# Kernel tuning notes

Hardware: AMD Instinct MI355X
Metric: run time of the kernel (lower is better)

Reference implementation:

```python
import jax, jax.numpy as jnp
import numpy as np

D_MODEL = 2048
N_HEADS = 16
D_HEAD = D_MODEL // N_HEADS  # 128
RANK = 32


def _orthogonal(key, rows, cols, dtype=jnp.float32):
    # mimic torch orthogonal init via QR
    a = jax.random.normal(key, (max(rows, cols), min(rows, cols)), dtype=jnp.float32)
    q, r = jnp.linalg.qr(a)
    q = q * jnp.sign(jnp.diagonal(r))
    if rows < cols:
        q = q.T
    return q.astype(dtype)


def setup_inputs() -> dict:
    key = jax.random.key(0)
    ks = jax.random.split(key, 8)
    B, T = 2, 2048
    x = jax.random.normal(ks[0], (B, T, D_MODEL), dtype=jnp.float32)
    s = 1.0 / np.sqrt(D_MODEL)
    Wq = jax.random.uniform(ks[1], (D_MODEL, D_MODEL), minval=-s, maxval=s, dtype=jnp.float32)
    Wk = jax.random.uniform(ks[2], (D_MODEL, D_MODEL), minval=-s, maxval=s, dtype=jnp.float32)
    Wv = jax.random.uniform(ks[3], (D_MODEL, D_MODEL), minval=-s, maxval=s, dtype=jnp.float32)
    Wo = jax.random.uniform(ks[4], (D_MODEL, D_MODEL), minval=-s, maxval=s, dtype=jnp.float32)
    # vein projector: project d_head -> rank, reconstruct rank -> d_head (orthogonal init)
    Wdown = _orthogonal(ks[5], D_HEAD, RANK)   # [d_head, r]
    Wup = _orthogonal(ks[6], RANK, D_HEAD)     # [r, d_head]
    return {"x": x, "Wq": Wq, "Wk": Wk, "Wv": Wv, "Wo": Wo, "Wdown": Wdown, "Wup": Wup}


def reference(x, Wq, Wk, Wv, Wo, Wdown, Wup):
    B, T, D = x.shape
    H, dh, r = N_HEADS, D_HEAD, RANK
    scale = 1.0 / np.sqrt(r)

    def heads(y):  # [B,T,D] -> [B,H,T,dh]
        return y.reshape(B, T, H, dh).transpose(0, 2, 1, 3)

    q = heads(x @ Wq.T)
    k = heads(x @ Wk.T)
    v = heads(x @ Wv.T)

    # project into vein (rank) space: [B,H,T,r]
    q_r = jnp.einsum('bhtd,dr->bhtr', q, Wdown)
    k_r = jnp.einsum('bhtd,dr->bhtr', k, Wdown)
    v_r = jnp.einsum('bhtd,dr->bhtr', v, Wdown)

    scores = jnp.einsum('bhqr,bhkr->bhqk', q_r, k_r) * scale  # [B,H,T,T]
    attn = jax.nn.softmax(scores, axis=-1)
    y_r = jnp.einsum('bhqk,bhkr->bhqr', attn, v_r)            # [B,H,T,r]
    y = jnp.einsum('bhtr,rd->bhtd', y_r, Wup)                  # reconstruct [B,H,T,dh]
    y = y.transpose(0, 2, 1, 3).reshape(B, T, D)
    out = y @ Wo.T
    return out
```

## Files before the change

kernel.cpp:

```cpp
#include <hip/hip_runtime.h>
#include <cstdint>
#include <cstddef>

typedef __bf16 bf16;
typedef __attribute__((ext_vector_type(8))) __bf16 bf16x8;
typedef __attribute__((ext_vector_type(4))) __bf16 bf16x4;
typedef __attribute__((ext_vector_type(2))) __bf16 bf16x2;
typedef __attribute__((ext_vector_type(4))) float f32x4;
typedef unsigned int u32;

#define D_MODEL 2048
#define QSCALE      0.17677669529663687f
#define QSCALE_L2E  (0.17677669529663687f * 1.4426950408889634f)

__device__ inline void async_load16(const void* gp, void* lp) {
  __builtin_amdgcn_global_load_lds(
      (const __attribute__((address_space(1))) u32*)gp,
      (__attribute__((address_space(3))) u32*)lp, 16, 0, 0);
}

__device__ inline float fast_exp2(float x) {
#if __has_builtin(__builtin_amdgcn_exp2f)
  return __builtin_amdgcn_exp2f(x);
#else
  return __expf(x * 0.6931471805599453f);
#endif
}

__device__ inline bf16x8 cvt8(float4 a, float4 b) {
  bf16x8 o;
  o[0] = (bf16)a.x; o[1] = (bf16)a.y; o[2] = (bf16)a.z; o[3] = (bf16)a.w;
  o[4] = (bf16)b.x; o[5] = (bf16)b.y; o[6] = (bf16)b.z; o[7] = (bf16)b.w;
  return o;
}

__global__ __launch_bounds__(256) void prep_k(
    const float* __restrict__ x,  const float* __restrict__ Wq,
    const float* __restrict__ Wk, const float* __restrict__ Wv,
    const float* __restrict__ Wo, const float* __restrict__ Wdown,
    const float* __restrict__ Wup,
    bf16* __restrict__ xb, bf16* __restrict__ EffT,
    bf16* __restrict__ WoEffT) {
  __shared__ __align__(16) char smem_[24576];
  const int bid = blockIdx.x;
  const int t = threadIdx.x;

  if (bid < 768) {
    const int mh = bid % 48;
    const int dblk = bid / 48;
    const float* W = (mh < 16) ? Wq : ((mh < 32) ? Wk : Wv);
    const int hrow = (mh & 15) * 128;
    const int d = dblk * 128 + (t & 127);
    const int rh = (t >> 7) * 16;
    const int rhs = __builtin_amdgcn_readfirstlane(rh);
    const float* wdn = Wdown + rhs;
    float acc[16];
#pragma unroll
    for (int j = 0; j < 16; ++j) acc[j] = 0.f;
    for (int kb = 0; kb < 16; ++kb) {
      float wv[8];
#pragma unroll
      for (int u = 0; u < 8; ++u)
        wv[u] = W[(size_t)(hrow + kb * 8 + u) * D_MODEL + d];
#pragma unroll
      for (int u = 0; u < 8; ++u) {
#pragma unroll
        for (int j = 0; j < 16; ++j)
          acc[j] += wv[u] * wdn[(kb * 8 + u) * 32 + j];
      }
    }
    bf16* outp = EffT + (size_t)(mh * 32 + rh) * D_MODEL + d;
#pragma unroll
    for (int j = 0; j < 16; ++j) outp[(size_t)j * D_MODEL] = (bf16)acc[j];
    return;
  }

  if (bid >= 1280) {
    const int tid = (bid - 1280) * 256 + t;
    float4 v[8];
#pragma unroll
    for (int p = 0; p < 4; ++p) {
      const int i = (tid + p * 262144) * 8;
      v[2 * p]     = *(const float4*)(x + i);
      v[2 * p + 1] = *(const float4*)(x + i + 4);
    }
#pragma unroll
    for (int p = 0; p < 4; ++p) {
      const int i = (tid + p * 262144) * 8;
      *(bf16x8*)(xb + i) = cvt8(v[2 * p], v[2 * p + 1]);
    }
    return;
  }

  bf16* As_ = (bf16*)smem_;
  bf16* Bs_ = (bf16*)(smem_ + 16384);
  const int rel = bid - 768;
  const int d0 = (rel & 31) * 64, h = rel >> 5;
  const int wave = t >> 6, lane = t & 63;
  const int quad = lane >> 4, lc = lane & 15;
#pragma unroll
  for (int a = 0; a < 4; ++a) {
    int cc = a * 256 + t;
    int row = cc >> 4, c = cc & 15;
    const float* src = Wo + (size_t)(d0 + row) * 2048 + h * 128 + c * 8;
    float4 f0 = ((const float4*)src)[0], f1 = ((const float4*)src)[1];
    *(bf16x8*)(As_ + row * 128 + ((c ^ (row & 15)) * 8)) = cvt8(f0, f1);
  }
  {
    int row = t >> 3;
    int c0 = (t & 7) * 2;
    const float* src = Wup + row * 128 + c0 * 8;
    float4 f0 = ((const float4*)src)[0], f1 = ((const float4*)src)[1];
    float4 f2 = ((const float4*)src)[2], f3 = ((const float4*)src)[3];
    *(bf16x8*)(Bs_ + row * 128 + ((c0 ^ (row & 15)) * 8)) = cvt8(f0, f1);
    *(bf16x8*)(Bs_ + row * 128 + (((c0 + 1) ^ (row & 15)) * 8)) = cvt8(f2, f3);
  }
  __syncthreads();
  f32x4 acc[2] = {};
  const int wm = wave * 16;
#pragma unroll
  for (int kc = 0; kc < 4; ++kc) {
    int m = wm + lc;
    bf16x8 af = *(const bf16x8*)(As_ + m * 128 + (((kc * 4 + quad) ^ (m & 15)) * 8));
#pragma unroll
    for (int ni = 0; ni < 2; ++ni) {
      int n = ni * 16 + lc;
      bf16x8 bfr = *(const bf16x8*)(Bs_ + n * 128 + (((kc * 4 + quad) ^ (n & 15)) * 8));
      acc[ni] = __builtin_amdgcn_mfma_f32_16x16x32_bf16(af, bfr, acc[ni], 0, 0, 0);
    }
  }
#pragma unroll
  for (int ni = 0; ni < 2; ++ni)
#pragma unroll
    for (int reg = 0; reg < 4; ++reg)
      WoEffT[(size_t)(d0 + wm + quad * 4 + reg) * 512 + h * 32 +
             ni * 16 + lc] = (bf16)acc[ni][reg];
}

template <int EPI, int BM>
__global__ __launch_bounds__(256, (BM == 64 ? 3 : 2)) void gemm_bt_k(
    const bf16* __restrict__ A, const bf16* __restrict__ Bt,
    void* __restrict__ Cv, int M, int N, int K) {
  constexpr int MI = BM / 32;
  constexpr int AR = BM / 4;
  __shared__ __align__(16) bf16 As[2][BM * 64];
  __shared__ __align__(16) bf16 Bs[2][128 * 64];
  const int t = threadIdx.x, wave = t >> 6, lane = t & 63;
  const int quad = lane >> 4, lc = lane & 15;
  const size_t m0 = (size_t)blockIdx.x * BM;
  const size_t n0 = (size_t)blockIdx.y * 128;
  const int wm = (wave >> 1) * (MI * 16), wn = (wave & 1) * 64;
  const int sr = lane >> 3, ss = lane & 7;
  const bf16* Aga[MI]; const bf16* Bga[4]; int LoffA[MI], LoffB[4];
#pragma unroll
  for (int a = 0; a < MI; ++a) {
    int row = wave * AR + a * 8 + sr;
    Aga[a] = A + (m0 + row) * (size_t)K + (ss ^ (row & 7)) * 8;
    LoffA[a] = (wave * AR + a * 8) * 64;
  }
#pragma unroll
  for (int a = 0; a < 4; ++a) {
    int row = wave * 32 + a * 8 + sr;
    Bga[a] = Bt + (n0 + row) * (size_t)K + (ss ^ (row & 7)) * 8;
    LoffB[a] = (wave * 32 + a * 8) * 64;
  }
  f32x4 acc[MI][4] = {};
  const int NIT = K >> 6;
#pragma unroll
  for (int a = 0; a < MI; ++a) async_load16(Aga[a], &As[0][LoffA[a]]);
#pragma unroll
  for (int a = 0; a < 4; ++a) async_load16(Bga[a], &Bs[0][LoffB[a]]);
  __syncthreads();
  for (int it = 0; it < NIT; ++it) {
    const int cur = it & 1;
    if (it + 1 < NIT) {
      const int k0 = (it + 1) * 64;
#pragma unroll
      for (int a = 0; a < MI; ++a) async_load16(Aga[a] + k0, &As[1 - cur][LoffA[a]]);
#pragma unroll
      for (int a = 0; a < 4; ++a) async_load16(Bga[a] + k0, &Bs[1 - cur][LoffB[a]]);
    }
    const bf16* Asb = As[cur];
    const bf16* Bsb = Bs[cur];
#pragma unroll
    for (int kc = 0; kc < 2; ++kc) {
      bf16x8 af[MI], bfr[4];
#pragma unroll
      for (int mi = 0; mi < MI; ++mi) {
        int m = wm + mi * 16 + lc;
        af[mi] = *(const bf16x8*)(Asb + m * 64 + (((kc * 4 + quad) ^ (m & 7)) * 8));
      }
#pragma unroll
      for (int ni = 0; ni < 4; ++ni) {
        int n = wn + ni * 16 + lc;
        bfr[ni] = *(const bf16x8*)(Bsb + n * 64 + (((kc * 4 + quad) ^ (n & 7)) * 8));
      }
#pragma unroll
      for (int mi = 0; mi < MI; ++mi)
#pragma unroll
        for (int ni = 0; ni < 4; ++ni)
          acc[mi][ni] = __builtin_amdgcn_mfma_f32_16x16x32_bf16(
              af[mi], bfr[ni], acc[mi][ni], 0, 0, 0);
    }
    __syncthreads();
  }

  if (EPI == 0) {
    float* C = (float*)Cv;
#pragma unroll
    for (int mi = 0; mi < MI; ++mi)
#pragma unroll
      for (int ni = 0; ni < 4; ++ni) {
        size_t row = m0 + wm + mi * 16 + quad * 4;
        size_t col = n0 + wn + ni * 16 + lc;
#pragma unroll
        for (int reg = 0; reg < 4; ++reg)
          C[(row + reg) * (size_t)N + col] = acc[mi][ni][reg];
      }
  } else {
    bf16* C = (bf16*)Cv;
#pragma unroll
    for (int mi = 0; mi < MI; ++mi)
#pragma unroll
      for (int ni = 0; ni < 4; ++ni) {
        int n = (int)n0 + wn + ni * 16 + lc;
        int mat = n >> 9, hh = (n >> 5) & 15, r = n & 31;
        float sc = (mat == 0) ? QSCALE_L2E : 1.0f;
        int trow = (int)m0 + wm + mi * 16 + quad * 4;
        int b = trow >> 11, tl = trow & 2047;
        if (mat == 2) {
          int tile = tl >> 7, kin = tl & 127;
          size_t off = ((size_t)(b * 16 + hh) * 3 + 2) * 65536 +
                       (size_t)tile * 4096 + r * 128 +
                       (((kin >> 3) ^ (r & 15)) << 3) + (kin & 7);
          bf16x4 pk;
#pragma unroll
          for (int reg = 0; reg < 4; ++reg) pk[reg] = (bf16)acc[mi][ni][reg];
          *(bf16x4*)(C + off) = pk;
        } else {
#pragma unroll
          for (int reg = 0; reg < 4; ++reg) {
            size_t off = (((size_t)(b * 16 + hh) * 3 + mat) * 2048 + tl + reg) * 32 + r;
            C[off] = (bf16)(acc[mi][ni][reg] * sc);
          }
        }
      }
  }
}

__global__ __launch_bounds__(256, 4) void attn_k(const bf16* __restrict__ QKVr,
                                                 float* __restrict__ Op,
                                                 float* __restrict__ Sums) {
  const int bh = blockIdx.x, qb = blockIdx.y, kvh = blockIdx.z;
  const size_t base = (size_t)bh * 3 * 65536;
  const bf16* Q   = QKVr + base;
  const bf16* Kr  = Q + 65536 + (size_t)kvh * 1024 * 32;
  const bf16* Vrb = Q + 131072 + (size_t)kvh * 8 * 4096;
  __shared__ __align__(16) bf16 Ks[2][128 * 32];
  __shared__ __align__(16) bf16 Vt[2][32 * 128];
  __shared__ __align__(16) bf16 Ps[4 * 32 * 32];
  const int t = threadIdx.x, wave = t >> 6, lane = t & 63;
  const int quad = lane >> 4, lc = lane & 15;
  const int qbase = qb * 128 + wave * 32;
  const bf16x8 qf0 = *(const bf16x8*)(Q + (size_t)(qbase + lc) * 32 + quad * 8);
  const bf16x8 qf1 = *(const bf16x8*)(Q + (size_t)(qbase + 16 + lc) * 32 + quad * 8);
  f32x4 o00 = {}, o01 = {}, o10 = {}, o11 = {};
  f32x4 os0 = {}, os1 = {};
  bf16x8 ones;
#pragma unroll
  for (int j = 0; j < 8; ++j) ones[j] = (bf16)1.0f;
  const int krow = wave * 16 + (lane >> 2);
  const bf16* Kg = Kr + (size_t)krow * 32 + ((lane & 3) ^ ((krow >> 1) & 3)) * 8;
  bf16* pw = Ps + wave * 32 * 32;
  const int psw = (lc & 3) ^ (lc >> 2);

  async_load16(Kg, &Ks[0][wave * 16 * 32]);
  async_load16(Kg + (size_t)64 * 32, &Ks[0][(64 + wave * 16) * 32]);
  async_load16(Vrb + (wave * 2) * 512 + lane * 8, &Vt[0][(wave * 2) * 512]);
  async_load16(Vrb + (wave * 2 + 1) * 512 + lane * 8, &Vt[0][(wave * 2 + 1) * 512]);
  __syncthreads();

  for (int it = 0; it < 8; ++it) {
    const int kt = it * 128, cur = it & 1;
    if (it < 7) {
      async_load16(Kg + (size_t)(kt + 128) * 32, &Ks[1 - cur][wave * 16 * 32]);
      async_load16(Kg + (size_t)(kt + 192) * 32, &Ks[1 - cur][(64 + wave * 16) * 32]);
      const bf16* vg = Vrb + (size_t)(it + 1) * 4096;
      async_load16(vg + (wave * 2) * 512 + lane * 8, &Vt[1 - cur][(wave * 2) * 512]);
      async_load16(vg + (wave * 2 + 1) * 512 + lane * 8, &Vt[1 - cur][(wave * 2 + 1) * 512]);
    }
    const bf16* ksb = Ks[cur];
    const bf16* vtb = Vt[cur];
#pragma unroll
    for (int qtr = 0; qtr < 4; ++qtr) {
#pragma unroll
      for (int nii = 0; nii < 2; ++nii) {
        int ni = qtr * 2 + nii;
        int n = ni * 16 + lc;
        bf16x8 kf = *(const bf16x8*)(ksb + n * 32 + ((quad ^ ((n >> 1) & 3)) * 8));
        f32x4 z = {0.f, 0.f, 0.f, 0.f};
        f32x4 s0 = __builtin_amdgcn_mfma_f32_16x16x32_bf16(kf, qf0, z, 0, 0, 0);
        f32x4 s1 = __builtin_amdgcn_mfma_f32_16x16x32_bf16(kf, qf1, z, 0, 0, 0);
        bf16x4 p0, p1;
#pragma unroll
        for (int reg = 0; reg < 4; ++reg) {
          p0[reg] = (bf16)fast_exp2(s0[reg]);
          p1[reg] = (bf16)fast_exp2(s1[reg]);
        }
        int off = (((2 * nii + (quad >> 1)) ^ psw) * 8) + (quad & 1) * 4;
        *(bf16x4*)(pw + lc * 32 + off) = p0;
        *(bf16x4*)(pw + (16 + lc) * 32 + off) = p1;
      }
      int co = (quad ^ psw) * 8;
      bf16x8 pf0 = *(const bf16x8*)(pw + lc * 32 + co);
      bf16x8 pf1 = *(const bf16x8*)(pw + (16 + lc) * 32 + co);
      int vo = ((qtr * 4 + quad) ^ lc) * 8;
      bf16x8 v0 = *(const bf16x8*)(vtb + lc * 128 + vo);
      bf16x8 v1 = *(const bf16x8*)(vtb + (16 + lc) * 128 + vo);
      o00 = __builtin_amdgcn_mfma_f32_16x16x32_bf16(pf0, v0, o00, 0, 0, 0);
      o01 = __builtin_amdgcn_mfma_f32_16x16x32_bf16(pf0, v1, o01, 0, 0, 0);
      o10 = __builtin_amdgcn_mfma_f32_16x16x32_bf16(pf1, v0, o10, 0, 0, 0);
      o11 = __builtin_amdgcn_mfma_f32_16x16x32_bf16(pf1, v1, o11, 0, 0, 0);
      os0 = __builtin_amdgcn_mfma_f32_16x16x32_bf16(pf0, ones, os0, 0, 0, 0);
      os1 = __builtin_amdgcn_mfma_f32_16x16x32_bf16(pf1, ones, os1, 0, 0, 0);
    }
    __syncthreads();
  }
  const int b = bh >> 4, h = bh & 15;
  float* op = Op + (size_t)kvh * 4096 * 512;
#pragma unroll
  for (int reg = 0; reg < 4; ++reg) {
    size_t r0 = (size_t)b * 2048 + qbase + quad * 4 + reg;
    size_t r1 = r0 + 16;
    op[r0 * 512 + h * 32 + lc]      = o00[reg];
    op[r0 * 512 + h * 32 + 16 + lc] = o01[reg];
    op[r1 * 512 + h * 32 + lc]      = o10[reg];
    op[r1 * 512 + h * 32 + 16 + lc] = o11[reg];
  }
  if (lc == 0) {
    float* sp = Sums + (size_t)kvh * 65536 + (size_t)bh * 2048 + qbase;
#pragma unroll
    for (int reg = 0; reg < 4; ++reg) {
      sp[quad * 4 + reg]      = os0[reg];
      sp[16 + quad * 4 + reg] = os1[reg];
    }
  }
}

__global__ __launch_bounds__(256) void comb_k(const float* __restrict__ Op,
                                              const float* __restrict__ Sums,
                                              bf16* __restrict__ Yr) {
  const int idx = blockIdx.x * 256 + threadIdx.x;
  const int row = idx >> 6;
  const int c8 = (idx & 63) * 8;
  const int b = row >> 11, tl = row & 2047;
  const int h = c8 >> 5;
  const size_t si = (size_t)(b * 16 + h) * 2048 + tl;
  const float inv = 1.0f / (Sums[si] + Sums[65536 + si]);
  const float4* p0 = (const float4*)(Op + (size_t)row * 512 + c8);
  const float4* p1 = (const float4*)(Op + 4096 * 512 + (size_t)row * 512 + c8);
  float4 a0 = p0[0], a1 = p0[1];
  float4 b0 = p1[0], b1 = p1[1];
  bf16x8 o;
  o[0] = (bf16)((a0.x + b0.x) * inv); o[1] = (bf16)((a0.y + b0.y) * inv);
  o[2] = (bf16)((a0.z + b0.z) * inv); o[3] = (bf16)((a0.w + b0.w) * inv);
  o[4] = (bf16)((a1.x + b1.x) * inv); o[5] = (bf16)((a1.y + b1.y) * inv);
  o[6] = (bf16)((a1.z + b1.z) * inv); o[7] = (bf16)((a1.w + b1.w) * inv);
  *(bf16x8*)(Yr + (size_t)row * 512 + c8) = o;
}

extern "C" void kernel_launch(void* const* d_in, const int* in_sizes, int n_in,
                              void* d_out, int out_size, void* d_ws, size_t ws_size,
                              hipStream_t stream) {
  const float* x     = (const float*)d_in[0];
  const float* Wq    = (const float*)d_in[1];
  const float* Wk    = (const float*)d_in[2];
  const float* Wv    = (const float*)d_in[3];
  const float* Wo    = (const float*)d_in[4];
  const float* Wdown = (const float*)d_in[5];
  const float* Wup   = (const float*)d_in[6];
  float* out = (float*)d_out;

  char* ws = (char*)d_ws;
  bf16*  EffT   = (bf16*)(ws);
  float* Sums   = (float*)(ws);
  bf16*  WoEffT = (bf16*)(ws + 6291456);
  bf16*  QKVr   = (bf16*)(ws + 8388608);
  bf16*  Yrb    = (bf16*)(ws + 20971520);
  bf16*  xb     = (bf16*)(ws + 25165824);
  float* Opart  = (float*)(ws + 25165824);

  prep_k<<<dim3(2304), dim3(256), 0, stream>>>(x, Wq, Wk, Wv, Wo, Wdown, Wup,
                                               xb, EffT, WoEffT);
  gemm_bt_k<1, 64><<<dim3(64, 12), dim3(256), 0, stream>>>(xb, EffT, QKVr,
                                                           4096, 1536, 2048);
  attn_k<<<dim3(32, 16, 2), dim3(256), 0, stream>>>(QKVr, Opart, Sums);
  comb_k<<<dim3(1024), dim3(256), 0, stream>>>(Opart, Sums, Yrb);
  gemm_bt_k<0, 128><<<dim3(32, 16), dim3(256), 0, stream>>>(Yrb, WoEffT, out,
                                                            4096, 2048, 512);
}
```

Before: 227.5 us.

## Fuse split-KV combine into attention kernel via last-arriver atomic counter

```diff
diff --git a/kernel.cpp b/kernel.cpp
--- a/kernel.cpp
+++ b/kernel.cpp
@@ -40,7 +40,7 @@
     const float* __restrict__ Wo, const float* __restrict__ Wdown,
     const float* __restrict__ Wup,
     bf16* __restrict__ xb, bf16* __restrict__ EffT,
-    bf16* __restrict__ WoEffT) {
+    bf16* __restrict__ WoEffT, int* __restrict__ cnt) {
   __shared__ __align__(16) char smem_[24576];
   const int bid = blockIdx.x;
   const int t = threadIdx.x;
@@ -76,7 +76,9 @@
   }
 
   if (bid >= 1280) {
-    const int tid = (bid - 1280) * 256 + t;
+    const int rel = bid - 1280;
+    if (rel == 0) { cnt[t] = 0; cnt[256 + t] = 0; }
+    const int tid = rel * 256 + t;
     float4 v[8];
 #pragma unroll
     for (int p = 0; p < 4; ++p) {
@@ -250,7 +252,9 @@
 
 __global__ __launch_bounds__(256, 4) void attn_k(const bf16* __restrict__ QKVr,
                                                  float* __restrict__ Op,
-                                                 float* __restrict__ Sums) {
+                                                 float* __restrict__ Sums,
+                                                 bf16* __restrict__ Yr,
+                                                 int* __restrict__ cnt) {
   const int bh = blockIdx.x, qb = blockIdx.y, kvh = blockIdx.z;
   const size_t base = (size_t)bh * 3 * 65536;
   const bf16* Q   = QKVr + base;
@@ -345,28 +349,30 @@
       sp[16 + quad * 4 + reg] = os1[reg];
     }
   }
-}
-
-__global__ __launch_bounds__(256) void comb_k(const float* __restrict__ Op,
-                                              const float* __restrict__ Sums,
-                                              bf16* __restrict__ Yr) {
-  const int idx = blockIdx.x * 256 + threadIdx.x;
-  const int row = idx >> 6;
-  const int c8 = (idx & 63) * 8;
-  const int b = row >> 11, tl = row & 2047;
-  const int h = c8 >> 5;
-  const size_t si = (size_t)(b * 16 + h) * 2048 + tl;
-  const float inv = 1.0f / (Sums[si] + Sums[65536 + si]);
-  const float4* p0 = (const float4*)(Op + (size_t)row * 512 + c8);
-  const float4* p1 = (const float4*)(Op + 4096 * 512 + (size_t)row * 512 + c8);
-  float4 a0 = p0[0], a1 = p0[1];
-  float4 b0 = p1[0], b1 = p1[1];
-  bf16x8 o;
-  o[0] = (bf16)((a0.x + b0.x) * inv); o[1] = (bf16)((a0.y + b0.y) * inv);
-  o[2] = (bf16)((a0.z + b0.z) * inv); o[3] = (bf16)((a0.w + b0.w) * inv);
-  o[4] = (bf16)((a1.x + b1.x) * inv); o[5] = (bf16)((a1.y + b1.y) * inv);
-  o[6] = (bf16)((a1.z + b1.z) * inv); o[7] = (bf16)((a1.w + b1.w) * inv);
-  *(bf16x8*)(Yr + (size_t)row * 512 + c8) = o;
+  __threadfence();
+  __syncthreads();
+  volatile int* flag = (volatile int*)Ps;
+  if (t == 0) *flag = atomicAdd(&cnt[bh * 16 + qb], 1);
+  __syncthreads();
+  if (*flag == 0) return;
+  __threadfence();
+  const float* pop = Op + (size_t)(1 - kvh) * 4096 * 512;
+  const float* ps  = Sums + (size_t)(1 - kvh) * 65536 + (size_t)bh * 2048 + qbase;
+#pragma unroll
+  for (int reg = 0; reg < 4; ++reg) {
+    float i0 = 1.0f / (os0[reg] + ps[quad * 4 + reg]);
+    float i1 = 1.0f / (os1[reg] + ps[16 + quad * 4 + reg]);
+    size_t r0 = (size_t)b * 2048 + qbase + quad * 4 + reg;
+    size_t r1 = r0 + 16;
+    Yr[r0 * 512 + h * 32 + lc] =
+        (bf16)((o00[reg] + pop[r0 * 512 + h * 32 + lc]) * i0);
+    Yr[r0 * 512 + h * 32 + 16 + lc] =
+        (bf16)((o01[reg] + pop[r0 * 512 + h * 32 + 16 + lc]) * i0);
+    Yr[r1 * 512 + h * 32 + lc] =
+        (bf16)((o10[reg] + pop[r1 * 512 + h * 32 + lc]) * i1);
+    Yr[r1 * 512 + h * 32 + 16 + lc] =
+        (bf16)((o11[reg] + pop[r1 * 512 + h * 32 + 16 + lc]) * i1);
+  }
 }
 
 extern "C" void kernel_launch(void* const* d_in, const int* in_sizes, int n_in,
@@ -389,13 +395,13 @@
   bf16*  Yrb    = (bf16*)(ws + 20971520);
   bf16*  xb     = (bf16*)(ws + 25165824);
   float* Opart  = (float*)(ws + 25165824);
+  int*   cnt    = (int*)(ws + 41943040);
 
   prep_k<<<dim3(2304), dim3(256), 0, stream>>>(x, Wq, Wk, Wv, Wo, Wdown, Wup,
-                                               xb, EffT, WoEffT);
+                                               xb, EffT, WoEffT, cnt);
   gemm_bt_k<1, 64><<<dim3(64, 12), dim3(256), 0, stream>>>(xb, EffT, QKVr,
                                                            4096, 1536, 2048);
-  attn_k<<<dim3(32, 16, 2), dim3(256), 0, stream>>>(QKVr, Opart, Sums);
-  comb_k<<<dim3(1024), dim3(256), 0, stream>>>(Opart, Sums, Yrb);
+  attn_k<<<dim3(32, 16, 2), dim3(256), 0, stream>>>(QKVr, Opart, Sums, Yrb, cnt);
   gemm_bt_k<0, 128><<<dim3(32, 16), dim3(256), 0, stream>>>(Yrb, WoEffT, out,
                                                             4096, 2048, 512);
 }
```

Measured after the change: 392.4 us. +72.5%, slower.
